# Kernel tuning notes

Hardware: AMD Instinct MI355X
Metric: run time of the kernel (lower is better)

Reference implementation:

```python
import jax, jax.numpy as jnp
import numpy as np

N_LAST = 4096  # power of two; K=1 path of get_hadK


def fwht(x):
    """Fast Walsh-Hadamard transform along the last dim, normalized by 1/sqrt(n).
    Matches QuaRot matmul_hadU butterfly recursion (K=1, power-of-two n)."""
    n = x.shape[-1]
    y = x.reshape(-1, n, 1)  # (B, n, 1)
    while y.shape[1] > 1:
        y = y.reshape(y.shape[0], y.shape[1] // 2, 2, y.shape[2])
        a = y[:, :, 0, :]
        b = y[:, :, 1, :]
        # butterfly: interleave (a+b, a-b) back into the trailing dim
        y = jnp.concatenate([a + b, a - b], axis=-1)  # (B, m/2, 2k)
    return y.reshape(x.shape) * np.float32(1.0 / np.sqrt(n))


def setup_inputs() -> dict:
    key = jax.random.key(0)
    x = jax.random.normal(key, (4, 2048, N_LAST), dtype=jnp.float32)
    return {"x": x}


def reference(x) -> jnp.ndarray:
    # HadamardTransform.forward with do_rotate=True
    dtype = x.dtype
    return fwht(x).astype(dtype)
```

## Files before the change

kernel.cpp:

```cpp
#include <hip/hip_runtime.h>


constexpr int N = 4096;
constexpr int LDS_STRIDE = 17;

__device__ __forceinline__ void wht16(float v[16]) {
#pragma unroll
    for (int m = 1; m < 16; m <<= 1) {
#pragma unroll
        for (int g = 0; g < 16; g += 2 * m) {
#pragma unroll
            for (int k = 0; k < m; ++k) {
                float a = v[g + k];
                float b = v[g + k + m];
                v[g + k]     = a + b;
                v[g + k + m] = a - b;
            }
        }
    }
}

__global__ __launch_bounds__(256, 4) void fwht4096_kernel(const float* __restrict__ in,
                                                          float* __restrict__ out) {
    __shared__ float lds[256 * LDS_STRIDE];

    const int t = threadIdx.x;
    const size_t row = blockIdx.x;
    const float* __restrict__ src = in + row * (size_t)N;
    float* __restrict__ dst = out + row * (size_t)N;

    float v[16];

    {
        const float4* s4 = (const float4*)(src + t * 16);
        float4 f0 = s4[0], f1 = s4[1], f2 = s4[2], f3 = s4[3];
        v[0]=f0.x;  v[1]=f0.y;  v[2]=f0.z;  v[3]=f0.w;
        v[4]=f1.x;  v[5]=f1.y;  v[6]=f1.z;  v[7]=f1.w;
        v[8]=f2.x;  v[9]=f2.y;  v[10]=f2.z; v[11]=f2.w;
        v[12]=f3.x; v[13]=f3.y; v[14]=f3.z; v[15]=f3.w;
    }
    wht16(v);

    {
        const int base = (t >> 4) * (16 * LDS_STRIDE) + (t & 15);
#pragma unroll
        for (int j = 0; j < 16; ++j) lds[base + j * LDS_STRIDE] = v[j];
    }
    __syncthreads();
    {
        const int base = t * LDS_STRIDE;
#pragma unroll
        for (int p = 0; p < 16; ++p) v[p] = lds[base + p];
    }
    wht16(v);
    __syncthreads();

    {
        const int base = (t & 15) * LDS_STRIDE + (t >> 4);
#pragma unroll
        for (int j = 0; j < 16; ++j) lds[base + j * (16 * LDS_STRIDE)] = v[j];
    }
    __syncthreads();
    {
        const int base = t * LDS_STRIDE;
#pragma unroll
        for (int p = 0; p < 16; ++p) v[p] = lds[base + p];
    }
    wht16(v);

    const float scale = 0.015625f;
#pragma unroll
    for (int p = 0; p < 16; ++p) dst[p * 256 + t] = v[p] * scale;
}

extern "C" void kernel_launch(void* const* d_in, const int* in_sizes, int n_in,
                              void* d_out, int out_size, void* d_ws, size_t ws_size,
                              hipStream_t stream) {
    const float* x = (const float*)d_in[0];
    float* y = (float*)d_out;
    const int rows = in_sizes[0] / N;
    fwht4096_kernel<<<rows, 256, 0, stream>>>(x, y);
}
```

Baseline: 227.2 us.

## Make FWHT kernel persistent with next-row prefetch and double-buffered LDS

Launches a fixed 1024 blocks that each process 8 rows in a loop instead of one block per row. The next row's global load is issued into a separate register set while the current row's butterfly stages run, and two LDS buffers let the three barriers drop to two per row, using a raw waitcnt+barrier. This targets exposed load latency and per-block launch cost in a memory-bound kernel, in exchange for more registers and a row count hardcoded at 8192 that ignores the input size.

```diff
diff --git a/kernel.cpp b/kernel.cpp
--- a/kernel.cpp
+++ b/kernel.cpp
@@ -2,7 +2,11 @@
 
 
 constexpr int N = 4096;
-constexpr int LDS_STRIDE = 17;
+constexpr int S = 17;
+constexpr int NBLOCKS = 1024;
+constexpr int ROWS_PER_BLOCK = 8192 / NBLOCKS;
+
+#define BAR_LGKM() asm volatile("s_waitcnt lgkmcnt(0)\ns_barrier" ::: "memory")
 
 __device__ __forceinline__ void wht16(float v[16]) {
 #pragma unroll
@@ -20,57 +24,71 @@
     }
 }
 
+__device__ __forceinline__ void load16(float v[16], const float* __restrict__ p) {
+    const float4* s4 = (const float4*)p;
+    float4 f0 = s4[0], f1 = s4[1], f2 = s4[2], f3 = s4[3];
+    v[0]=f0.x;  v[1]=f0.y;  v[2]=f0.z;  v[3]=f0.w;
+    v[4]=f1.x;  v[5]=f1.y;  v[6]=f1.z;  v[7]=f1.w;
+    v[8]=f2.x;  v[9]=f2.y;  v[10]=f2.z; v[11]=f2.w;
+    v[12]=f3.x; v[13]=f3.y; v[14]=f3.z; v[15]=f3.w;
+}
+
+__device__ __forceinline__ void t1_write(float* lds, const float v[16], int t) {
+    const int base = (t >> 4) * (16 * S) + (t & 15);
+#pragma unroll
+    for (int j = 0; j < 16; ++j) lds[base + j * S] = v[j];
+}
+__device__ __forceinline__ void t2_write(float* lds, const float v[16], int t) {
+    const int base = (t & 15) * S + (t >> 4);
+#pragma unroll
+    for (int p = 0; p < 16; ++p) lds[base + p * (16 * S)] = v[p];
+}
+__device__ __forceinline__ void rd16(const float* lds, float v[16], int t) {
+    const int base = t * S;
+#pragma unroll
+    for (int p = 0; p < 16; ++p) v[p] = lds[base + p];
+}
+
 __global__ __launch_bounds__(256, 4) void fwht4096_kernel(const float* __restrict__ in,
                                                           float* __restrict__ out) {
-    __shared__ float lds[256 * LDS_STRIDE];
+    __shared__ float ldsA[256 * S];
+    __shared__ float ldsB[256 * S];
 
     const int t = threadIdx.x;
-    const size_t row = blockIdx.x;
-    const float* __restrict__ src = in + row * (size_t)N;
-    float* __restrict__ dst = out + row * (size_t)N;
+    size_t row = blockIdx.x;
+    const float scale = 0.015625f;
 
-    float v[16];
+    float v[16], pf[16];
+    load16(v, in + row * (size_t)N + t * 16);
 
-    {
-        const float4* s4 = (const float4*)(src + t * 16);
-        float4 f0 = s4[0], f1 = s4[1], f2 = s4[2], f3 = s4[3];
-        v[0]=f0.x;  v[1]=f0.y;  v[2]=f0.z;  v[3]=f0.w;
-        v[4]=f1.x;  v[5]=f1.y;  v[6]=f1.z;  v[7]=f1.w;
-        v[8]=f2.x;  v[9]=f2.y;  v[10]=f2.z; v[11]=f2.w;
-        v[12]=f3.x; v[13]=f3.y; v[14]=f3.z; v[15]=f3.w;
+#pragma unroll 1
+    for (int it = 0; it < ROWS_PER_BLOCK; ++it) {
+        const size_t nrow = row + NBLOCKS;
+        const bool has_next = (it + 1 < ROWS_PER_BLOCK);
+
+        wht16(v);
+        t1_write(ldsA, v, t);
+        if (has_next) load16(pf, in + nrow * (size_t)N + t * 16);
+        BAR_LGKM();
+
+        rd16(ldsA, v, t);
+        wht16(v);
+        t2_write(ldsB, v, t);
+        BAR_LGKM();
+
+        rd16(ldsB, v, t);
+        wht16(v);
+
+        float* __restrict__ dst = out + row * (size_t)N;
+#pragma unroll
+        for (int p = 0; p < 16; ++p) dst[p * 256 + t] = v[p] * scale;
+
+        if (has_next) {
+#pragma unroll
+            for (int q = 0; q < 16; ++q) v[q] = pf[q];
+            row = nrow;
+        }
     }
-    wht16(v);
-
-    {
-        const int base = (t >> 4) * (16 * LDS_STRIDE) + (t & 15);
-#pragma unroll
-        for (int j = 0; j < 16; ++j) lds[base + j * LDS_STRIDE] = v[j];
-    }
-    __syncthreads();
-    {
-        const int base = t * LDS_STRIDE;
-#pragma unroll
-        for (int p = 0; p < 16; ++p) v[p] = lds[base + p];
-    }
-    wht16(v);
-    __syncthreads();
-
-    {
-        const int base = (t & 15) * LDS_STRIDE + (t >> 4);
-#pragma unroll
-        for (int j = 0; j < 16; ++j) lds[base + j * (16 * LDS_STRIDE)] = v[j];
-    }
-    __syncthreads();
-    {
-        const int base = t * LDS_STRIDE;
-#pragma unroll
-        for (int p = 0; p < 16; ++p) v[p] = lds[base + p];
-    }
-    wht16(v);
-
-    const float scale = 0.015625f;
-#pragma unroll
-    for (int p = 0; p < 16; ++p) dst[p * 256 + t] = v[p] * scale;
 }
 
 extern "C" void kernel_launch(void* const* d_in, const int* in_sizes, int n_in,
@@ -78,6 +96,5 @@
                               hipStream_t stream) {
     const float* x = (const float*)d_in[0];
     float* y = (float*)d_out;
-    const int rows = in_sizes[0] / N;
-    fwht4096_kernel<<<rows, 256, 0, stream>>>(x, y);
+    fwht4096_kernel<<<NBLOCKS, 256, 0, stream>>>(x, y);
 }
```

After: 229.1 us. Within noise of the previous version (+0.9%).
